# Performance work log

Measured on AMD Instinct MI355X. Metric: run time of the kernel, lower is better.

## Reference

```python
import jax, jax.numpy as jnp
import numpy as np

B, T = 1024, 512
BN_EPS = 1e-5


def _lstm_dir(x, w_ih, w_hh, b, reverse=False):
    """Single-direction LSTM, PyTorch gate order (i, f, g, o).
    x: [B, T, D]; w_ih: [4H, D]; w_hh: [4H, H]; b: [4H]. Returns [B, T, H]."""
    if reverse:
        x = x[:, ::-1]
    xw = jnp.einsum('btd,gd->btg', x, w_ih) + b  # precompute input contribution [B,T,4H]
    H = w_hh.shape[1]
    h0 = jnp.zeros((x.shape[0], H), x.dtype)

    def step(carry, xw_t):
        h, c = carry
        g = xw_t + h @ w_hh.T
        i, f, gg, o = jnp.split(g, 4, axis=-1)
        c = jax.nn.sigmoid(f) * c + jax.nn.sigmoid(i) * jnp.tanh(gg)
        h = jax.nn.sigmoid(o) * jnp.tanh(c)
        return (h, c), h

    _, ys = jax.lax.scan(step, (h0, h0), jnp.swapaxes(xw, 0, 1))
    ys = jnp.swapaxes(ys, 0, 1)  # [B,T,H]
    if reverse:
        ys = ys[:, ::-1]
    return ys


def _bilstm(x, w_ih, w_hh, b):
    # w_ih: [2,4H,D] (dir 0 = forward, dir 1 = backward)
    return jnp.concatenate([
        _lstm_dir(x, w_ih[0], w_hh[0], b[0]),
        _lstm_dir(x, w_ih[1], w_hh[1], b[1], reverse=True),
    ], axis=-1)


def _pool2(x):
    # MaxPool1d(2) over time on channel-last layout: [B,T,C] -> [B,T//2,C]
    b, t, c = x.shape
    return x.reshape(b, t // 2, 2, c).max(axis=2)


def setup_inputs() -> dict:
    key = jax.random.key(0)
    ks = iter(jax.random.split(key, 32))
    s = 0.1  # small init to avoid gate saturation
    d = {}
    d['x'] = jax.random.normal(next(ks), (B, 11, T), jnp.float32)
    d['conv_w'] = jax.random.normal(next(ks), (64, 11), jnp.float32) * s
    d['conv_b'] = jax.random.normal(next(ks), (64,), jnp.float32) * s
    d['bn_gamma'] = jax.random.uniform(next(ks), (64,), jnp.float32, 0.5, 1.5)
    d['bn_beta'] = jax.random.normal(next(ks), (64,), jnp.float32) * s
    d['bn_mean'] = jax.random.normal(next(ks), (64,), jnp.float32) * s
    d['bn_var'] = jax.random.uniform(next(ks), (64,), jnp.float32, 0.5, 1.5)
    for name, shp in [
        ('l1_wih0', (2, 64, 64)), ('l1_whh0', (2, 64, 16)), ('l1_b0', (2, 64)),
        ('l1_wih1', (2, 64, 32)), ('l1_whh1', (2, 64, 16)), ('l1_b1', (2, 64)),
        ('l2_wih0', (2, 32, 32)), ('l2_whh0', (2, 32, 8)), ('l2_b0', (2, 32)),
        ('l2_wih1', (2, 32, 16)), ('l2_whh1', (2, 32, 8)), ('l2_b1', (2, 32)),
        ('l3_wih0', (2, 16, 16)), ('l3_whh0', (2, 16, 4)), ('l3_b0', (2, 16)),
    ]:
        d[name] = jax.random.normal(next(ks), shp, jnp.float32) * s
    return d


def reference(x, conv_w, conv_b, bn_gamma, bn_beta, bn_mean, bn_var,
              l1_wih0, l1_whh0, l1_b0, l1_wih1, l1_whh1, l1_b1,
              l2_wih0, l2_whh0, l2_b0, l2_wih1, l2_whh1, l2_b1,
              l3_wih0, l3_whh0, l3_b0):
    # conv1x1: [B,11,T] -> [B,64,T]
    y = jnp.einsum('bct,oc->bot', x, conv_w) + conv_b[:, None]
    # BatchNorm1d (inference, running stats), fused scale/shift
    inv = bn_gamma / jnp.sqrt(bn_var + BN_EPS)
    y = (y - bn_mean[:, None]) * inv[:, None] + bn_beta[:, None]
    y = jnp.swapaxes(y, 1, 2)                      # [B,T,64]
    y = _bilstm(y, l1_wih0, l1_whh0, l1_b0)        # [B,T,32]
    y = _bilstm(y, l1_wih1, l1_whh1, l1_b1)        # [B,T,32]
    y = _pool2(y)                                  # [B,T/2,32]
    y = _bilstm(y, l2_wih0, l2_whh0, l2_b0)        # [B,T/2,16]
    y = _bilstm(y, l2_wih1, l2_whh1, l2_b1)        # [B,T/2,16]
    y = _pool2(y)                                  # [B,T/4,16]
    y = _bilstm(y, l3_wih0, l3_whh0, l3_b0)        # [B,T/4,8]
    return jnp.swapaxes(y, 1, 2)                   # [B,8,T/4]
```

## Files before the change

kernel.cpp:

```cpp
#include <hip/hip_runtime.h>

#define TB 128

typedef float v2f __attribute__((ext_vector_type(2)));
typedef _Float16 f16;
typedef _Float16 h2v __attribute__((ext_vector_type(2)));

__device__ __forceinline__ float rcp_f(float x) { return __builtin_amdgcn_rcpf(x); }
__device__ __forceinline__ float exp2_f(float x) { return __builtin_amdgcn_exp2f(x); }
__device__ __forceinline__ float dpp_xor2(float x) {
  return __int_as_float(__builtin_amdgcn_update_dpp(0, __float_as_int(x), 0x4E, 0xF, 0xF, true));
}
__device__ __forceinline__ float dpp_xor1(float x) {
  return __int_as_float(__builtin_amdgcn_update_dpp(0, __float_as_int(x), 0xB1, 0xF, 0xF, true));
}

#if __has_builtin(__builtin_amdgcn_fdot2)
__device__ __forceinline__ float fdot2(h2v a, h2v b, float c) {
  return __builtin_amdgcn_fdot2(a, b, c, false);
}
#else
__device__ __forceinline__ float fdot2(h2v a, h2v b, float c) {
  return fmaf((float)a.x, (float)b.x, fmaf((float)a.y, (float)b.y, c));
}
#endif

#define AM_G (-5.7707801636f)
#define AB_G (2.8853900818f)

template<int D, int H, int T, int INS, int OUTS, int DEPTH, bool HIN,
         bool POOL, bool TOUT, typename OutT, typename InT>
__device__ __forceinline__ void scan(const void* wv, const float* hr,
                                     float bb, float am, float ab,
                                     const InT* in, OutT* out,
                                     int dir, int wl, float* h_base) {
  constexpr int NF4 = HIN ? (D / 8) : (D / 4);
  constexpr int NH4 = H / 4;
  const int tau = wl & 3;
  const int j = (wl >> 2) & (H - 1);
  const bool st = (tau == 1) && ((wl >> 2) < H);
  if (wl < H) h_base[wl] = 0.f;
  __builtin_amdgcn_wave_barrier();
  float4 hreg[NH4];
#pragma unroll
  for (int i = 0; i < NH4; ++i) hreg[i] = *(const float4*)(h_base + 4 * i);
  __builtin_amdgcn_wave_barrier();

  int t = dir ? (T - 1) : 0;
  const int dt = dir ? -1 : 1;

  float4 bufs[DEPTH][NF4];
  auto ldin = [&](float4* dst, int tt) {
    tt = tt < 0 ? 0 : (tt > T - 1 ? T - 1 : tt);
    const float4* p = (const float4*)((const char*)in + (size_t)tt * INS * sizeof(InT));
#pragma unroll
    for (int i = 0; i < NF4; ++i) dst[i] = p[i];
  };
  auto xwdot = [&](const float4* b) -> float {
    if constexpr (HIN) {
      const h2v* hp = (const h2v*)b;
      const h2v* wh = (const h2v*)wv;
      float a0 = bb, a1 = 0.f, a2 = 0.f, a3 = 0.f;
#pragma unroll
      for (int i = 0; i < D / 2; i += 4) {
        a0 = fdot2(wh[i + 0], hp[i + 0], a0);
        a1 = fdot2(wh[i + 1], hp[i + 1], a1);
        a2 = fdot2(wh[i + 2], hp[i + 2], a2);
        a3 = fdot2(wh[i + 3], hp[i + 3], a3);
      }
      return (a0 + a1) + (a2 + a3);
    } else {
      const float* c = (const float*)b;
      const float* wr = (const float*)wv;
      v2f q0 = {bb, 0.f}, q1 = {0.f, 0.f};
#pragma unroll
      for (int i = 0; i < D; i += 4) {
        q0 = __builtin_elementwise_fma(*(const v2f*)(wr + i), *(const v2f*)(c + i), q0);
        q1 = __builtin_elementwise_fma(*(const v2f*)(wr + i + 2), *(const v2f*)(c + i + 2), q1);
      }
      v2f qs = q0 + q1;
      return qs.x + qs.y;
    }
  };

#pragma unroll
  for (int k = 0; k < DEPTH; ++k) ldin(bufs[k], t + k * dt);
  float xw = xwdot(bufs[0]);
  float cs = 0.f, pm = 0.f;

  for (int s = 0; s < T; s += DEPTH) {
#pragma unroll
    for (int k = 0; k < DEPTH; ++k) {
      v2f r0 = {xw, 0.f}, r1 = {0.f, 0.f};
#pragma unroll
      for (int i = 0; i < NH4; ++i) {
        r0 = __builtin_elementwise_fma(*(const v2f*)(hr + 4 * i), (v2f){hreg[i].x, hreg[i].y}, r0);
        r1 = __builtin_elementwise_fma(*(const v2f*)(hr + 4 * i + 2), (v2f){hreg[i].z, hreg[i].w}, r1);
      }
      v2f rs = r0 + r1;
      float acc = rs.x + rs.y;
      float sg = rcp_f(1.f + exp2_f(-acc));
      float a = fmaf(am, sg, ab);
      float b = dpp_xor2(a);
      float p = a * b;
      float q = dpp_xor1(p);
      float fv = (tau == 1) ? a : b;
      float ov = (tau == 1) ? b : a;
      cs = fmaf(fv, cs, q);
      float th = fmaf(2.f, rcp_f(1.f + exp2_f(cs)), -1.f);
      float hv = ov * th;
      if (st) h_base[j] = hv;
      __builtin_amdgcn_wave_barrier();
#pragma unroll
      for (int i = 0; i < NH4; ++i) hreg[i] = *(const float4*)(h_base + 4 * i);
      xw = xwdot(bufs[(k + 1) % DEPTH]);
      ldin(bufs[k], t + DEPTH * dt);
      if (st) {
        if constexpr (TOUT) {
          out[(dir * H + j) * T + t] = (OutT)hv;
        } else if constexpr (POOL) {
          if (k & 1) out[(t >> 1) * OUTS + dir * H + j] = (OutT)fmaxf(pm, hv);
          else pm = hv;
        } else {
          out[t * OUTS + dir * H + j] = (OutT)hv;
        }
      }
      __builtin_amdgcn_wave_barrier();
      t += dt;
    }
  }
}

template<int D, int H>
__device__ __forceinline__ void load_wbh(const float* __restrict__ wih,
                                         const float* __restrict__ whh,
                                         const float* __restrict__ bias,
                                         int dir, int wl,
                                         h2v* wh, float* hr, float& bb,
                                         float& am, float& ab) {
  constexpr float L2E = 1.4426950408889634f;
  const int tau = wl & 3;
  const int j = (wl >> 2) & (H - 1);
  const bool isg = (tau == 2);
  const float k = isg ? 2.f * L2E : L2E;
  am = isg ? AM_G : 1.f;
  ab = isg ? AB_G : 0.f;
  const int row = dir * 4 * H + tau * H + j;
  const float* p = wih + row * D;
#pragma unroll
  for (int i = 0; i < D / 2; ++i)
    wh[i] = (h2v){(f16)(p[2 * i] * k), (f16)(p[2 * i + 1] * k)};
  const float* q = whh + row * H;
#pragma unroll
  for (int i = 0; i < H; ++i) hr[i] = q[i] * k;
  bb = bias[row] * k;
}

__global__ __launch_bounds__(TB) void lstm_all(
    const float* __restrict__ x,
    const float* __restrict__ conv_w, const float* __restrict__ conv_b,
    const float* __restrict__ bn_g, const float* __restrict__ bn_b,
    const float* __restrict__ bn_m, const float* __restrict__ bn_v,
    const float* __restrict__ w1a_ih, const float* __restrict__ w1a_hh, const float* __restrict__ b1a,
    const float* __restrict__ w1b_ih, const float* __restrict__ w1b_hh, const float* __restrict__ b1b,
    const float* __restrict__ w2a_ih, const float* __restrict__ w2a_hh, const float* __restrict__ b2a,
    const float* __restrict__ w2b_ih, const float* __restrict__ w2b_hh, const float* __restrict__ b2b,
    const float* __restrict__ w3_ih, const float* __restrict__ w3_hh, const float* __restrict__ b3,
    float* __restrict__ out, f16* __restrict__ ws, int row0) {
  const int row = row0 + blockIdx.x;
  const int tid = threadIdx.x;
  const int wave = tid >> 6;
  const int lane = tid & 63;

  __shared__ __align__(16) char R1[24576];
  __shared__ __align__(16) f16 A2h[256 * 16];
  __shared__ __align__(16) float w2c[64][11];
  __shared__ float b2c[64];
  __shared__ __align__(16) float hb[32];

  float (*xs)[12] = (float(*)[12])R1;
  f16* LBh = (f16*)R1;
  f16* LB2h = (f16*)(R1 + 16384);
  f16* Ah = ws + (size_t)blockIdx.x * 16384;

  const float* xrow = x + (size_t)row * 5632;
  for (int i = tid; i < 5632; i += TB) {
    int c = i >> 9, t = i & 511;
    xs[t][c] = xrow[i];
  }
  for (int i = tid; i < 512; i += TB) xs[i][11] = 0.f;
  if (tid < 64) {
    float inv = bn_g[tid] * rsqrtf(bn_v[tid] + 1e-5f);
    for (int c = 0; c < 11; ++c) w2c[tid][c] = conv_w[tid * 11 + c] * inv;
    b2c[tid] = fmaf(conv_b[tid] - bn_m[tid], inv, bn_b[tid]);
  }
  __syncthreads();

  {
    constexpr float L2E = 1.4426950408889634f;
    const int tau = lane & 3;
    const int j = lane >> 2;
    const int row_l = wave * 64 + tau * 16 + j;
    float weff[12], beff;
#pragma unroll
    for (int c = 0; c < 12; ++c) weff[c] = 0.f;
    const float* wih = w1a_ih + row_l * 64;
    beff = b1a[row_l];
    for (int d = 0; d < 64; ++d) {
      float wd = wih[d];
      beff = fmaf(wd, b2c[d], beff);
#pragma unroll
      for (int c = 0; c < 11; ++c) weff[c] = fmaf(wd, w2c[d][c], weff[c]);
    }
    const bool isg = (tau == 2);
    const float k = isg ? 2.f * L2E : L2E;
#pragma unroll
    for (int c = 0; c < 12; ++c) weff[c] *= k;
    beff *= k;
    float am = isg ? AM_G : 1.f, ab = isg ? AB_G : 0.f;
    float hrw[16];
    const float* q = w1a_hh + row_l * 16;
#pragma unroll
    for (int i = 0; i < 16; ++i) hrw[i] = q[i] * k;
    if (wave) __builtin_amdgcn_s_sleep(4);
    scan<12, 16, 512, 12, 32, 2, false, false, false, f16, float>(
        weff, hrw, beff, am, ab, &xs[0][0], Ah, wave, lane, hb + wave * 16);
  }
  __syncthreads();

  {
    h2v wh[16]; float hr[16], bb, am, ab;
    load_wbh<32, 16>(w1b_ih, w1b_hh, b1b, wave, lane, wh, hr, bb, am, ab);
    if (wave) __builtin_amdgcn_s_sleep(4);
    scan<32, 16, 512, 32, 32, 4, true, true, false, f16, f16>(
        wh, hr, bb, am, ab, Ah, LBh, wave, lane, hb + wave * 16);
  }
  __syncthreads();

  if (wave == 0) {
    const int dir = lane >> 5, wl = lane & 31;
    h2v wh[16]; float hr[8], bb, am, ab;
    load_wbh<32, 8>(w2a_ih, w2a_hh, b2a, dir, wl, wh, hr, bb, am, ab);
    scan<32, 8, 256, 32, 16, 2, true, false, false, f16, f16>(
        wh, hr, bb, am, ab, LBh, A2h, dir, wl, hb + dir * 16);
  }
  __syncthreads();

  if (wave == 0) {
    const int dir = lane >> 5, wl = lane & 31;
    h2v wh[8]; float hr[8], bb, am, ab;
    load_wbh<16, 8>(w2b_ih, w2b_hh, b2b, dir, wl, wh, hr, bb, am, ab);
    scan<16, 8, 256, 16, 16, 2, true, true, false, f16, f16>(
        wh, hr, bb, am, ab, A2h, LB2h, dir, wl, hb + dir * 16);
  }
  __syncthreads();

  if (wave == 0) {
    const int dir = lane >> 5, wl = lane & 31;
    h2v wh[8]; float hr[4], bb, am, ab;
    load_wbh<16, 4>(w3_ih, w3_hh, b3, dir, wl, wh, hr, bb, am, ab);
    scan<16, 4, 128, 16, 8, 2, true, false, true, float, f16>(
        wh, hr, bb, am, ab, LB2h, out + (size_t)row * 1024, dir, wl, hb + dir * 16);
  }
}

extern "C" void kernel_launch(void* const* d_in, const int* in_sizes, int n_in,
                              void* d_out, int out_size, void* d_ws, size_t ws_size,
                              hipStream_t stream) {
  const float* x      = (const float*)d_in[0];
  const float* conv_w = (const float*)d_in[1];
  const float* conv_b = (const float*)d_in[2];
  const float* bn_g   = (const float*)d_in[3];
  const float* bn_b   = (const float*)d_in[4];
  const float* bn_m   = (const float*)d_in[5];
  const float* bn_v   = (const float*)d_in[6];
  const float* w1a_ih = (const float*)d_in[7];
  const float* w1a_hh = (const float*)d_in[8];
  const float* b1a    = (const float*)d_in[9];
  const float* w1b_ih = (const float*)d_in[10];
  const float* w1b_hh = (const float*)d_in[11];
  const float* b1b    = (const float*)d_in[12];
  const float* w2a_ih = (const float*)d_in[13];
  const float* w2a_hh = (const float*)d_in[14];
  const float* b2a    = (const float*)d_in[15];
  const float* w2b_ih = (const float*)d_in[16];
  const float* w2b_hh = (const float*)d_in[17];
  const float* b2b    = (const float*)d_in[18];
  const float* w3_ih  = (const float*)d_in[19];
  const float* w3_hh  = (const float*)d_in[20];
  const float* b3     = (const float*)d_in[21];

  const size_t per_row_bytes = 16384 * sizeof(f16);
  int rows_per = (int)(ws_size / per_row_bytes);
  if (rows_per < 1) rows_per = 1;
  if (rows_per > 1024) rows_per = 1024;

  for (int r0 = 0; r0 < 1024; r0 += rows_per) {
    int n = 1024 - r0;
    if (n > rows_per) n = rows_per;
    lstm_all<<<n, TB, 0, stream>>>(x, conv_w, conv_b, bn_g, bn_b, bn_m, bn_v,
                                   w1a_ih, w1a_hh, b1a, w1b_ih, w1b_hh, b1b,
                                   w2a_ih, w2a_hh, b2a, w2b_ih, w2b_hh, b2b,
                                   w3_ih, w3_hh, b3,
                                   (float*)d_out, (f16*)d_ws, r0);
  }
}
```

Before: 372.9 us.

## Store recurrent state and weights in fp16 and use fdot2 for recurrence

Recurrent hidden state in LDS and the hh weights move to packed fp16, so the per-step recurrent matvec uses fdot2 instead of fp32 FMAs, and the hidden-state reload takes fewer LDS bytes. The first layer's input is staged as fp16 padded to 16 channels so it can share the fp16 input-dot path. The time loop peels the last DEPTH steps, which drops the clamp on prefetch indices. This shortens the serial per-step critical path at the cost of lower precision in the recurrence.

```diff
diff --git a/kernel.cpp b/kernel.cpp
--- a/kernel.cpp
+++ b/kernel.cpp
@@ -30,20 +30,30 @@
 
 template<int D, int H, int T, int INS, int OUTS, int DEPTH, bool HIN,
          bool POOL, bool TOUT, typename OutT, typename InT>
-__device__ __forceinline__ void scan(const void* wv, const float* hr,
+__device__ __forceinline__ void scan(const void* wv, const h2v* hrh,
                                      float bb, float am, float ab,
                                      const InT* in, OutT* out,
-                                     int dir, int wl, float* h_base) {
+                                     int dir, int wl, f16* h16) {
   constexpr int NF4 = HIN ? (D / 8) : (D / 4);
-  constexpr int NH4 = H / 4;
+  constexpr int NHW = H / 2;
   const int tau = wl & 3;
   const int j = (wl >> 2) & (H - 1);
   const bool st = (tau == 1) && ((wl >> 2) < H);
-  if (wl < H) h_base[wl] = 0.f;
+  if (wl < H) h16[wl] = (f16)0.f;
   __builtin_amdgcn_wave_barrier();
-  float4 hreg[NH4];
-#pragma unroll
-  for (int i = 0; i < NH4; ++i) hreg[i] = *(const float4*)(h_base + 4 * i);
+
+  h2v hreg[NHW];
+  auto ldh = [&]() {
+    if constexpr (H == 16) {
+      *(float4*)&hreg[0] = *(const float4*)(h16);
+      *(float4*)&hreg[4] = *(const float4*)(h16 + 8);
+    } else if constexpr (H == 8) {
+      *(float4*)&hreg[0] = *(const float4*)(h16);
+    } else {
+      *(float2*)&hreg[0] = *(const float2*)(h16);
+    }
+  };
+  ldh();
   __builtin_amdgcn_wave_barrier();
 
   int t = dir ? (T - 1) : 0;
@@ -51,7 +61,6 @@
 
   float4 bufs[DEPTH][NF4];
   auto ldin = [&](float4* dst, int tt) {
-    tt = tt < 0 ? 0 : (tt > T - 1 ? T - 1 : tt);
     const float4* p = (const float4*)((const char*)in + (size_t)tt * INS * sizeof(InT));
 #pragma unroll
     for (int i = 0; i < NF4; ++i) dst[i] = p[i];
@@ -88,47 +97,49 @@
   float xw = xwdot(bufs[0]);
   float cs = 0.f, pm = 0.f;
 
-  for (int s = 0; s < T; s += DEPTH) {
-#pragma unroll
-    for (int k = 0; k < DEPTH; ++k) {
-      v2f r0 = {xw, 0.f}, r1 = {0.f, 0.f};
-#pragma unroll
-      for (int i = 0; i < NH4; ++i) {
-        r0 = __builtin_elementwise_fma(*(const v2f*)(hr + 4 * i), (v2f){hreg[i].x, hreg[i].y}, r0);
-        r1 = __builtin_elementwise_fma(*(const v2f*)(hr + 4 * i + 2), (v2f){hreg[i].z, hreg[i].w}, r1);
+  auto body = [&](int k, bool reload) {
+    float a0 = xw, a1 = 0.f;
+#pragma unroll
+    for (int i = 0; i < NHW; i += 2) {
+      a0 = fdot2(hrh[i], hreg[i], a0);
+      if (i + 1 < NHW) a1 = fdot2(hrh[i + 1], hreg[i + 1], a1);
+    }
+    float acc = a0 + a1;
+    float sg = rcp_f(1.f + exp2_f(-acc));
+    float a = fmaf(am, sg, ab);
+    float b = dpp_xor2(a);
+    float p = a * b;
+    float q = dpp_xor1(p);
+    float fv = (tau == 1) ? a : b;
+    float ov = (tau == 1) ? b : a;
+    cs = fmaf(fv, cs, q);
+    float th = fmaf(2.f, rcp_f(1.f + exp2_f(cs)), -1.f);
+    float hv = ov * th;
+    if (st) h16[j] = (f16)hv;
+    __builtin_amdgcn_wave_barrier();
+    ldh();
+    xw = xwdot(bufs[(k + 1) % DEPTH]);
+    if (reload) ldin(bufs[k], t + DEPTH * dt);
+    if (st) {
+      if constexpr (TOUT) {
+        out[(dir * H + j) * T + t] = (OutT)hv;
+      } else if constexpr (POOL) {
+        if (k & 1) out[(t >> 1) * OUTS + dir * H + j] = (OutT)fmaxf(pm, hv);
+        else pm = hv;
+      } else {
+        out[t * OUTS + dir * H + j] = (OutT)hv;
       }
-      v2f rs = r0 + r1;
-      float acc = rs.x + rs.y;
-      float sg = rcp_f(1.f + exp2_f(-acc));
-      float a = fmaf(am, sg, ab);
-      float b = dpp_xor2(a);
-      float p = a * b;
-      float q = dpp_xor1(p);
-      float fv = (tau == 1) ? a : b;
-      float ov = (tau == 1) ? b : a;
-      cs = fmaf(fv, cs, q);
-      float th = fmaf(2.f, rcp_f(1.f + exp2_f(cs)), -1.f);
-      float hv = ov * th;
-      if (st) h_base[j] = hv;
-      __builtin_amdgcn_wave_barrier();
-#pragma unroll
-      for (int i = 0; i < NH4; ++i) hreg[i] = *(const float4*)(h_base + 4 * i);
-      xw = xwdot(bufs[(k + 1) % DEPTH]);
-      ldin(bufs[k], t + DEPTH * dt);
-      if (st) {
-        if constexpr (TOUT) {
-          out[(dir * H + j) * T + t] = (OutT)hv;
-        } else if constexpr (POOL) {
-          if (k & 1) out[(t >> 1) * OUTS + dir * H + j] = (OutT)fmaxf(pm, hv);
-          else pm = hv;
-        } else {
-          out[t * OUTS + dir * H + j] = (OutT)hv;
-        }
-      }
-      __builtin_amdgcn_wave_barrier();
-      t += dt;
-    }
-  }
+    }
+    __builtin_amdgcn_wave_barrier();
+    t += dt;
+  };
+
+  for (int so = 0; so < T / DEPTH - 1; ++so) {
+#pragma unroll
+    for (int k = 0; k < DEPTH; ++k) body(k, true);
+  }
+#pragma unroll
+  for (int k = 0; k < DEPTH; ++k) body(k, false);
 }
 
 template<int D, int H>
@@ -136,7 +147,7 @@
                                          const float* __restrict__ whh,
                                          const float* __restrict__ bias,
                                          int dir, int wl,
-                                         h2v* wh, float* hr, float& bb,
+                                         h2v* wh, h2v* hrh, float& bb,
                                          float& am, float& ab) {
   constexpr float L2E = 1.4426950408889634f;
   const int tau = wl & 3;
@@ -152,7 +163,8 @@
     wh[i] = (h2v){(f16)(p[2 * i] * k), (f16)(p[2 * i + 1] * k)};
   const float* q = whh + row * H;
 #pragma unroll
-  for (int i = 0; i < H; ++i) hr[i] = q[i] * k;
+  for (int i = 0; i < H / 2; ++i)
+    hrh[i] = (h2v){(f16)(q[2 * i] * k), (f16)(q[2 * i + 1] * k)};
   bb = bias[row] * k;
 }
 
@@ -172,13 +184,13 @@
   const int wave = tid >> 6;
   const int lane = tid & 63;
 
-  __shared__ __align__(16) char R1[24576];
+  __shared__ __align__(16) char R1[20480];
   __shared__ __align__(16) f16 A2h[256 * 16];
   __shared__ __align__(16) float w2c[64][11];
   __shared__ float b2c[64];
-  __shared__ __align__(16) float hb[32];
-
-  float (*xs)[12] = (float(*)[12])R1;
+  __shared__ __align__(16) f16 hb16[2][16];
+
+  f16 (*xs16)[16] = (f16(*)[16])R1;
   f16* LBh = (f16*)R1;
   f16* LB2h = (f16*)(R1 + 16384);
   f16* Ah = ws + (size_t)blockIdx.x * 16384;
@@ -186,9 +198,12 @@
   const float* xrow = x + (size_t)row * 5632;
   for (int i = tid; i < 5632; i += TB) {
     int c = i >> 9, t = i & 511;
-    xs[t][c] = xrow[i];
-  }
-  for (int i = tid; i < 512; i += TB) xs[i][11] = 0.f;
+    xs16[t][c] = (f16)xrow[i];
+  }
+  for (int i = tid; i < 512 * 5; i += TB) {
+    int t = i / 5, c = 11 + i % 5;
+    xs16[t][c] = (f16)0.f;
+  }
   if (tid < 64) {
     float inv = bn_g[tid] * rsqrtf(bn_v[tid] + 1e-5f);
     for (int c = 0; c < 11; ++c) w2c[tid][c] = conv_w[tid * 11 + c] * inv;
@@ -201,11 +216,11 @@
     const int tau = lane & 3;
     const int j = lane >> 2;
     const int row_l = wave * 64 + tau * 16 + j;
-    float weff[12], beff;
-#pragma unroll
-    for (int c = 0; c < 12; ++c) weff[c] = 0.f;
+    float weff[16];
+#pragma unroll
+    for (int c = 0; c < 16; ++c) weff[c] = 0.f;
     const float* wih = w1a_ih + row_l * 64;
-    beff = b1a[row_l];
+    float beff = b1a[row_l];
     for (int d = 0; d < 64; ++d) {
       float wd = wih[d];
       beff = fmaf(wd, b2c[d], beff);
@@ -214,53 +229,56 @@
     }
     const bool isg = (tau == 2);
     const float k = isg ? 2.f * L2E : L2E;
-#pragma unroll
-    for (int c = 0; c < 12; ++c) weff[c] *= k;
     beff *= k;
+    h2v weffh[8];
+#pragma unroll
+    for (int i = 0; i < 8; ++i)
+      weffh[i] = (h2v){(f16)(weff[2 * i] * k), (f16)(weff[2 * i + 1] * k)};
     float am = isg ? AM_G : 1.f, ab = isg ? AB_G : 0.f;
-    float hrw[16];
+    h2v hrh[8];
     const float* q = w1a_hh + row_l * 16;
 #pragma unroll
-    for (int i = 0; i < 16; ++i) hrw[i] = q[i] * k;
+    for (int i = 0; i < 8; ++i)
+      hrh[i] = (h2v){(f16)(q[2 * i] * k), (f16)(q[2 * i + 1] * k)};
     if (wave) __builtin_amdgcn_s_sleep(4);
-    scan<12, 16, 512, 12, 32, 2, false, false, false, f16, float>(
-        weff, hrw, beff, am, ab, &xs[0][0], Ah, wave, lane, hb + wave * 16);
+    scan<16, 16, 512, 16, 32, 2, true, false, false, f16, f16>(
+        weffh, hrh, beff, am, ab, &xs16[0][0], Ah, wave, lane, hb16[wave]);
   }
   __syncthreads();
 
   {
-    h2v wh[16]; float hr[16], bb, am, ab;
-    load_wbh<32, 16>(w1b_ih, w1b_hh, b1b, wave, lane, wh, hr, bb, am, ab);
+    h2v wh[16]; h2v hrh[8]; float bb, am, ab;
+    load_wbh<32, 16>(w1b_ih, w1b_hh, b1b, wave, lane, wh, hrh, bb, am, ab);
     if (wave) __builtin_amdgcn_s_sleep(4);
     scan<32, 16, 512, 32, 32, 4, true, true, false, f16, f16>(
-        wh, hr, bb, am, ab, Ah, LBh, wave, lane, hb + wave * 16);
+        wh, hrh, bb, am, ab, Ah, LBh, wave, lane, hb16[wave]);
   }
   __syncthreads();
 
   if (wave == 0) {
     const int dir = lane >> 5, wl = lane & 31;
-    h2v wh[16]; float hr[8], bb, am, ab;
-    load_wbh<32, 8>(w2a_ih, w2a_hh, b2a, dir, wl, wh, hr, bb, am, ab);
+    h2v wh[16]; h2v hrh[4]; float bb, am, ab;
+    load_wbh<32, 8>(w2a_ih, w2a_hh, b2a, dir, wl, wh, hrh, bb, am, ab);
     scan<32, 8, 256, 32, 16, 2, true, false, false, f16, f16>(
-        wh, hr, bb, am, ab, LBh, A2h, dir, wl, hb + dir * 16);
+        wh, hrh, bb, am, ab, LBh, A2h, dir, wl, hb16[dir]);
   }
   __syncthreads();
 
   if (wave == 0) {
     const int dir = lane >> 5, wl = lane & 31;
-    h2v wh[8]; float hr[8], bb, am, ab;
-    load_wbh<16, 8>(w2b_ih, w2b_hh, b2b, dir, wl, wh, hr, bb, am, ab);
+    h2v wh[8]; h2v hrh[4]; float bb, am, ab;
+    load_wbh<16, 8>(w2b_ih, w2b_hh, b2b, dir, wl, wh, hrh, bb, am, ab);
     scan<16, 8, 256, 16, 16, 2, true, true, false, f16, f16>(
-        wh, hr, bb, am, ab, A2h, LB2h, dir, wl, hb + dir * 16);
+        wh, hrh, bb, am, ab, A2h, LB2h, dir, wl, hb16[dir]);
   }
   __syncthreads();
 
   if (wave == 0) {
     const int dir = lane >> 5, wl = lane & 31;
-    h2v wh[8]; float hr[4], bb, am, ab;
-    load_wbh<16, 4>(w3_ih, w3_hh, b3, dir, wl, wh, hr, bb, am, ab);
+    h2v wh[8]; h2v hrh[2]; float bb, am, ab;
+    load_wbh<16, 4>(w3_ih, w3_hh, b3, dir, wl, wh, hrh, bb, am, ab);
     scan<16, 4, 128, 16, 8, 2, true, false, true, float, f16>(
-        wh, hr, bb, am, ab, LB2h, out + (size_t)row * 1024, dir, wl, hb + dir * 16);
+        wh, hrh, bb, am, ab, LB2h, out + (size_t)row * 1024, dir, wl, hb16[dir]);
   }
 }
 
```

After: 385.2 us. 3.3% more time.
